# Optimization experiments

Hardware: AMD Instinct MI355X
Metric: run time of the kernel (lower is better)

The kernel has to match this reference:

```python
import jax, jax.numpy as jnp
import numpy as np

N_NODES = 50000
N_EDGES = 800000
IN_CH = 128
HEADS = 4
OUT_CH = 4
N_GRAPHS = 64
NEG_SLOPE = 0.2  # GATv2Conv default leaky_relu slope
EPS = 1e-5       # GraphNorm eps


def _seg_sum(x, seg, n):
    return jax.ops.segment_sum(x, seg, num_segments=n)


def _seg_mean(x, seg, n):
    s = _seg_sum(x, seg, n)
    cnt = _seg_sum(jnp.ones((seg.shape[0],), x.dtype), seg, n)
    return s / jnp.maximum(cnt, 1.0)[:, None]


def gatv2_conv(x, src, dst, n, w_l, w_r, att, bias, heads, out_ch, concat):
    # x: [N, F_in]; src/dst: [E_tot] (self-loops already appended)
    x_l = (x @ w_l).reshape(n, heads, out_ch)
    x_r = (x @ w_r).reshape(n, heads, out_ch)
    m = jax.nn.leaky_relu(x_l[src] + x_r[dst], NEG_SLOPE)   # [E, H, C]
    e = jnp.einsum('ehc,hc->eh', m, att)                    # [E, H]
    # softmax over incoming edges of each destination node
    e_max = jax.ops.segment_max(e, dst, num_segments=n)     # [N, H]
    w = jnp.exp(e - e_max[dst])
    denom = _seg_sum(w, dst, n)                             # [N, H]
    alpha = w / denom[dst]
    out = _seg_sum(alpha[:, :, None] * x_l[src], dst, n)    # [N, H, C]
    out = out.reshape(n, heads * out_ch) if concat else out.mean(axis=1)
    return out + bias


def graph_norm(x, batch, weight, bias, mean_scale, n_graphs):
    mu = _seg_mean(x, batch, n_graphs)                      # [G, C]
    out = x - mu[batch] * mean_scale
    var = _seg_mean(out * out, batch, n_graphs)
    return out / jnp.sqrt(var[batch] + EPS) * weight + bias


def setup_inputs() -> dict:
    key = jax.random.key(0)
    ks = jax.random.split(key, 20)
    H = HEADS
    d = {}
    d['x'] = jax.random.normal(ks[0], (N_NODES, IN_CH), dtype=jnp.float32)
    d['edge_index'] = jax.random.randint(ks[1], (2, N_EDGES), 0, N_NODES, dtype=jnp.int32)
    d['batch'] = jnp.sort(jax.random.randint(ks[2], (N_NODES,), 0, N_GRAPHS, dtype=jnp.int32))
    def glorot(k, shape):
        fan = shape[0] + shape[-1]
        return jax.random.normal(k, shape, dtype=jnp.float32) * np.sqrt(2.0 / fan).astype(np.float32)
    # layer 1: in 128 -> 32 per head, concat -> 128
    d['w_l1'] = glorot(ks[3], (IN_CH, H * 32)); d['w_r1'] = glorot(ks[4], (IN_CH, H * 32))
    d['att1'] = glorot(ks[5], (H, 32)); d['b1'] = jnp.zeros((H * 32,), jnp.float32)
    d['gn1_w'] = jnp.ones((H * 32,), jnp.float32); d['gn1_b'] = jnp.zeros((H * 32,), jnp.float32); d['gn1_s'] = jnp.ones((H * 32,), jnp.float32)
    # layer 2: 128 -> 16 per head, concat -> 64
    d['w_l2'] = glorot(ks[6], (H * 32, H * 16)); d['w_r2'] = glorot(ks[7], (H * 32, H * 16))
    d['att2'] = glorot(ks[8], (H, 16)); d['b2'] = jnp.zeros((H * 16,), jnp.float32)
    d['gn2_w'] = jnp.ones((H * 16,), jnp.float32); d['gn2_b'] = jnp.zeros((H * 16,), jnp.float32); d['gn2_s'] = jnp.ones((H * 16,), jnp.float32)
    # layer 3: 64 -> 8 per head, mean over heads -> 8
    d['w_l3'] = glorot(ks[9], (H * 16, H * 8)); d['w_r3'] = glorot(ks[10], (H * 16, H * 8))
    d['att3'] = glorot(ks[11], (H, 8)); d['b3'] = jnp.zeros((8,), jnp.float32)
    d['gn3_w'] = jnp.ones((8,), jnp.float32); d['gn3_b'] = jnp.zeros((8,), jnp.float32); d['gn3_s'] = jnp.ones((8,), jnp.float32)
    d['lin_w'] = glorot(ks[12], (8, OUT_CH)); d['lin_b'] = jnp.zeros((OUT_CH,), jnp.float32)
    return d


def reference(x, edge_index, batch,
              w_l1, w_r1, att1, b1, gn1_w, gn1_b, gn1_s,
              w_l2, w_r2, att2, b2, gn2_w, gn2_b, gn2_s,
              w_l3, w_r3, att3, b3, gn3_w, gn3_b, gn3_s,
              lin_w, lin_b):
    n = x.shape[0]
    loop = jnp.arange(n, dtype=edge_index.dtype)
    src = jnp.concatenate([edge_index[0], loop])  # add_self_loops=True (PyG default)
    dst = jnp.concatenate([edge_index[1], loop])
    h = gatv2_conv(x, src, dst, n, w_l1, w_r1, att1, b1, HEADS, 32, True)
    h = jax.nn.relu(graph_norm(h, batch, gn1_w, gn1_b, gn1_s, N_GRAPHS))
    h = gatv2_conv(h, src, dst, n, w_l2, w_r2, att2, b2, HEADS, 16, True)
    h = jax.nn.relu(graph_norm(h, batch, gn2_w, gn2_b, gn2_s, N_GRAPHS))
    h = gatv2_conv(h, src, dst, n, w_l3, w_r3, att3, b3, HEADS, 8, False)
    h = jax.nn.relu(graph_norm(h, batch, gn3_w, gn3_b, gn3_s, N_GRAPHS))
    features = _seg_mean(h, batch, N_GRAPHS)  # global_mean_pool -> [G, 8]
    logits = features @ lin_w + lin_b         # [G, OUT_CH]
    return (logits, features)
```

## Files before the change

kernel.cpp:

```cpp
#include <hip/hip_runtime.h>
#include <hip/hip_fp16.h>
#include <math.h>

#define NN 50000
#define NE 800000
#define ET (NE + NN)
#define NG 64
#define H 4
#define NBK 196
#define CH 2048
#define SB ((ET + CH - 1) / CH)
#define GD ((NN + 63) / 64)

typedef _Float16 half8 __attribute__((ext_vector_type(8)));
typedef _Float16 half4 __attribute__((ext_vector_type(4)));
typedef _Float16 hv2 __attribute__((ext_vector_type(2)));
typedef float floatx4 __attribute__((ext_vector_type(4)));


template <int K, int M2>
__device__ __forceinline__ void wprep_fn(int chunk, const float* __restrict__ Wl, const float* __restrict__ Wr,
                                         _Float16* __restrict__ Wfrag) {
    constexpr int MTOT = 2 * M2, NT = MTOT / 16;
    if (chunk >= MTOT * K / 8) return;
    int lane = chunk & 63, tt = chunk >> 6;
    int t = tt % NT, kt = tt / NT;
    int n = t * 16 + (lane & 15);
    int kb = kt * 32 + (lane >> 4) * 8;
    const float* src = (n < M2) ? (Wl + n) : (Wr + (n - M2));
    half8 h;
#pragma unroll
    for (int j = 0; j < 8; ++j) h[j] = (_Float16)src[(size_t)(kb + j) * M2];
    *(half8*)(Wfrag + (size_t)chunk * 8) = h;
}


__global__ __launch_bounds__(256) void k_prep(const float* __restrict__ Wl1, const float* __restrict__ Wr1,
                                              const float* __restrict__ Wl2, const float* __restrict__ Wr2,
                                              const float* __restrict__ Wl3, const float* __restrict__ Wr3,
                                              _Float16* __restrict__ Wf1, _Float16* __restrict__ Wf2,
                                              _Float16* __restrict__ Wf3,
                                              const int* __restrict__ batch, int* __restrict__ bpos,
                                              const int* __restrict__ ei, int* __restrict__ bcnt) {
    int b = blockIdx.x, t = threadIdx.x;
    if (b < 16) { wprep_fn<128, 128>(b * 256 + t, Wl1, Wr1, Wf1); return; }
    if (b < 24) { wprep_fn<128, 64>((b - 16) * 256 + t, Wl2, Wr2, Wf2); return; }
    if (b < 26) { wprep_fn<64, 32>((b - 24) * 256 + t, Wl3, Wr3, Wf3); return; }
    if (b < 26 + NBK) {
        int i = (b - 26) * 256 + t;
        if (i >= NN) return;
        int cur = batch[i];
        int prev = (i == 0) ? -1 : batch[i - 1];
        for (int g = prev + 1; g <= cur; ++g) bpos[g] = i;
        if (i == NN - 1)
            for (int g = cur + 1; g <= NG; ++g) bpos[g] = NN;
        return;
    }
    __shared__ int hist[NBK];
    int b0 = b - 26 - NBK;
    for (int i = t; i < NBK; i += 256) hist[i] = 0;
    __syncthreads();
#pragma unroll
    for (int pass = 0; pass < CH / 256; ++pass) {
        int e = b0 * CH + pass * 256 + t;
        if (e < ET) {
            int d = (e < NE) ? ei[NE + e] : (e - NE);
            atomicAdd(&hist[d >> 8], 1);
        }
    }
    __syncthreads();
    if (t < NBK) bcnt[t * SB + b0] = hist[t];
}


template <typename AT, bool NORM>
__device__ __forceinline__ half8 load_a8(const AT* __restrict__ ap, const float* pa, const float* pb) {
    if constexpr (NORM) {
        half8 raw = *(const half8*)ap;
        half8 h;
#pragma unroll
        for (int j = 0; j < 8; ++j) {
            float y = fmaf((float)raw[j], pa[j], pb[j]);
            h[j] = (_Float16)fmaxf(y, 0.f);
        }
        return h;
    } else if constexpr (__is_same(AT, _Float16)) {
        return *(const half8*)ap;
    } else {
        const float4* p = (const float4*)ap;
        float4 a = p[0], b = p[1];
        half8 h;
        h[0] = (_Float16)a.x; h[1] = (_Float16)a.y; h[2] = (_Float16)a.z; h[3] = (_Float16)a.w;
        h[4] = (_Float16)b.x; h[5] = (_Float16)b.y; h[6] = (_Float16)b.z; h[7] = (_Float16)b.w;
        return h;
    }
}

template <int K, int M2, typename AT, bool NORM>
__device__ __forceinline__ void dualgemm_body(int blk, int tid, const AT* __restrict__ Ain,
                                              const _Float16* __restrict__ Wfrag,
                                              __half* __restrict__ Ol, __half* __restrict__ Or,
                                              const float* __restrict__ gsum, const float* __restrict__ gsq,
                                              const float* __restrict__ gw, const float* __restrict__ gbb,
                                              const float* __restrict__ gms,
                                              const int* __restrict__ bpos, const int* __restrict__ batch) {
    constexpr int MTOT = 2 * M2;
    constexpr int NT = MTOT / 16;
    constexpr int KT = K / 32;
    constexpr int PK = NORM ? K : 1;
    __shared__ float spab[2][8][PK];
    int wid = tid >> 6, lane = tid & 63;
    int q = lane >> 4, l15 = lane & 15;
    int r0 = blk * 64 + wid * 16;
    int arow = min(r0 + l15, NN - 1);
    const AT* ap = Ain + (size_t)arow * K + q * 8;
    const float *pa = nullptr, *pb = nullptr;
    if constexpr (NORM) {
        int rb = blk * 64;
        int g0 = batch[min(rb, NN - 1)];
        int g1 = batch[min(rb + 63, NN - 1)];
        int gspan = min(g1 - g0 + 1, 8);
        for (int i = tid; i < gspan * K; i += 256) {
            int gg = i / K, c = i - gg * K;
            int g = g0 + gg;
            float cg = fmaxf((float)(bpos[g + 1] - bpos[g]), 1.f);
            float mu = gsum[(size_t)g * K + c] / cg;
            float ex2 = gsq[(size_t)g * K + c] / cg;
            float s_ = gms[c];
            float var = ex2 - s_ * (2.f - s_) * mu * mu;
            float a = rsqrtf(var + 1e-5f) * gw[c];
            spab[0][gg][c] = a;
            spab[1][gg][c] = gbb[c] - mu * s_ * a;
        }
        __syncthreads();
        int gg = min(batch[arow] - g0, 7);
        pa = &spab[0][gg][q * 8];
        pb = &spab[1][gg][q * 8];
    }

    floatx4 acc[NT];
#pragma unroll
    for (int t = 0; t < NT; ++t) acc[t] = (floatx4){0.f, 0.f, 0.f, 0.f};

#pragma unroll
    for (int kt = 0; kt < KT; ++kt) {
        half8 a8 = load_a8<AT, NORM>(ap + kt * 32, pa + (NORM ? kt * 32 : 0), pb + (NORM ? kt * 32 : 0));
        const _Float16* wp = Wfrag + ((size_t)(kt * NT) * 64 + lane) * 8;
#pragma unroll
        for (int t = 0; t < NT; ++t) {
            half8 b8 = *(const half8*)(wp + (size_t)t * 64 * 8);
            acc[t] = __builtin_amdgcn_mfma_f32_16x16x32_f16(a8, b8, acc[t], 0, 0, 0);
        }
    }

#pragma unroll
    for (int t = 0; t < NT; ++t) {
        int cn = t * 16 + l15;
#pragma unroll
        for (int reg = 0; reg < 4; ++reg) {
            int r = r0 + q * 4 + reg;
            if (r < NN) {
                if (cn < M2) Ol[(size_t)r * M2 + cn] = __float2half(acc[t][reg]);
                else         Or[(size_t)r * M2 + (cn - M2)] = __float2half(acc[t][reg]);
            }
        }
    }
}

template <int K, int M2>
__global__ __launch_bounds__(256) void k_dualgemm_n(const __half* __restrict__ Ain,
                                                    const _Float16* __restrict__ Wfrag,
                                                    __half* __restrict__ Ol, __half* __restrict__ Or,
                                                    const float* __restrict__ gsum, const float* __restrict__ gsq,
                                                    const float* __restrict__ gw, const float* __restrict__ gbb,
                                                    const float* __restrict__ gms,
                                                    const int* __restrict__ bpos, const int* __restrict__ batch) {
    dualgemm_body<K, M2, _Float16, true>(blockIdx.x, threadIdx.x, (const _Float16*)Ain, Wfrag, Ol, Or,
                                         gsum, gsq, gw, gbb, gms, bpos, batch);
}


__device__ __forceinline__ void bscanA_fn(int b, int t, const int* __restrict__ bcnt,
                                          int* __restrict__ boff, int* __restrict__ tot) {
    __shared__ int lds[256];
    int i0 = 2 * t, i1 = 2 * t + 1;
    int v0 = (i0 < SB) ? bcnt[b * SB + i0] : 0;
    int v1 = (i1 < SB) ? bcnt[b * SB + i1] : 0;
    int pair = v0 + v1;
    lds[t] = pair;
    __syncthreads();
    for (int off = 1; off < 256; off <<= 1) {
        int y = (t >= off) ? lds[t - off] : 0;
        __syncthreads();
        lds[t] += y;
        __syncthreads();
    }
    int excl = lds[t] - pair;
    if (i0 < SB) boff[b * SB + i0] = excl;
    if (i1 < SB) boff[b * SB + i1] = excl + v0;
    if (t == 255) tot[b] = lds[255];
}


__global__ __launch_bounds__(256) void k_gemm1_scan(const float* __restrict__ x, const _Float16* __restrict__ Wf1,
                                                    __half* __restrict__ Ol, __half* __restrict__ Or,
                                                    const int* __restrict__ bcnt, int* __restrict__ boff,
                                                    int* __restrict__ tot) {
    if (blockIdx.x < GD)
        dualgemm_body<128, 128, float, false>(blockIdx.x, threadIdx.x, x, Wf1, Ol, Or,
                                              nullptr, nullptr, nullptr, nullptr, nullptr, nullptr, nullptr);
    else
        bscanA_fn(blockIdx.x - GD, threadIdx.x, bcnt, boff, tot);
}


__device__ __forceinline__ void edge_sd(int e, const int* __restrict__ ei, int& s, int& d) {
    if (e < NE) { s = ei[e]; d = ei[NE + e]; } else { s = e - NE; d = s; }
}

__global__ __launch_bounds__(256) void k_bscatter(const int* __restrict__ ei, const int* __restrict__ tot,
                                                  const int* __restrict__ boff, unsigned int* __restrict__ ebuf) {
    __shared__ int eb[256];
    __shared__ int cur[NBK];
    int b0 = blockIdx.x, t = threadIdx.x;
    int v = (t < NBK) ? tot[t] : 0;
    eb[t] = v;
    __syncthreads();
    for (int off = 1; off < 256; off <<= 1) {
        int y = (t >= off) ? eb[t - off] : 0;
        __syncthreads();
        eb[t] += y;
        __syncthreads();
    }
    if (t < NBK) cur[t] = (eb[t] - v) + boff[t * SB + b0];
    __syncthreads();
#pragma unroll
    for (int pass = 0; pass < CH / 256; ++pass) {
        int e = b0 * CH + pass * 256 + t;
        if (e < ET) {
            int s, d;
            edge_sd(e, ei, s, d);
            int pos = atomicAdd(&cur[d >> 8], 1);
            ebuf[pos] = ((unsigned)s << 16) | (unsigned)(d & 255);
        }
    }
}


__global__ __launch_bounds__(256) void k_bsort(const unsigned int* __restrict__ ebuf,
                                               const int* __restrict__ tot,
                                               int* __restrict__ rowptr, unsigned short* __restrict__ colsrc) {
    __shared__ int eb[256];
    __shared__ int sbase;
    __shared__ int cnt2[256];
    __shared__ int sc[256];
    __shared__ int cur2[256];
    int b = blockIdx.x, t = threadIdx.x;
    int v = (t < NBK) ? tot[t] : 0;
    eb[t] = v;
    __syncthreads();
    for (int off = 1; off < 256; off <<= 1) {
        int y = (t >= off) ? eb[t - off] : 0;
        __syncthreads();
        eb[t] += y;
        __syncthreads();
    }
    if (t == b) sbase = eb[t] - v;
    __syncthreads();
    int base = sbase, n = tot[b];
    cnt2[t] = 0;
    __syncthreads();
    for (int i = t; i < n; i += 256) atomicAdd(&cnt2[ebuf[base + i] & 255], 1);
    __syncthreads();
    int cv = cnt2[t];
    sc[t] = cv;
    __syncthreads();
    for (int off = 1; off < 256; off <<= 1) {
        int y = (t >= off) ? sc[t - off] : 0;
        __syncthreads();
        sc[t] += y;
        __syncthreads();
    }
    int excl = sc[t] - cv;
    int d = b * 256 + t;
    if (d < NN) rowptr[d] = base + excl;
    if (b == 0 && t == 0) rowptr[NN] = ET;
    cur2[t] = excl;
    __syncthreads();
    for (int i = t; i < n; i += 256) {
        unsigned u = ebuf[base + i];
        int pos = atomicAdd(&cur2[u & 255], 1);
        colsrc[base + pos] = (unsigned short)(u >> 16);
    }
}


template <int CP> struct HVec { hv2 h2[CP / 2]; };

template <int CP>
__device__ __forceinline__ HVec<CP> load_hv(const __half* __restrict__ p) {
    HVec<CP> r;
    if constexpr (CP == 16) {
        float4* rp = (float4*)&r;
        rp[0] = ((const float4*)p)[0];
        rp[1] = ((const float4*)p)[1];
    } else if constexpr (CP == 8) {
        float4 t = *(const float4*)p; r = *(HVec<CP>*)&t;
    } else if constexpr (CP == 4) {
        float2 t = *(const float2*)p; r = *(HVec<CP>*)&t;
    } else {
        r.h2[0] = *(const hv2*)p;
    }
    return r;
}

template <int C, int EP, bool CONCAT>
__global__ __launch_bounds__(256) void k_attn(const __half* __restrict__ xl, const __half* __restrict__ xr,
                                              const int* __restrict__ rowptr,
                                              const unsigned short* __restrict__ colsrc,
                                              const float* __restrict__ att, const float* __restrict__ bias,
                                              __half* __restrict__ out) {
    constexpr int CP = C / EP;
    constexpr int LEP = (EP == 4) ? 2 : ((EP == 2) ? 1 : 0);
    int t = blockIdx.x * 256 + threadIdx.x;
    int part = t & (EP - 1);
    int nh = t >> LEP;
    if (nh >= NN * H) return;
    int node = nh >> 2, h = nh & 3;
    int cbase = h * C + part * CP;
    hv2 xrr2[CP / 2], attv2[CP / 2];
    float acc[CP];
    {
        HVec<CP> xrv = load_hv<CP>(xr + (size_t)node * (H * C) + cbase);
        const float* q = att + cbase;
#pragma unroll
        for (int j = 0; j < CP / 2; ++j) {
            xrr2[j] = xrv.h2[j];
            attv2[j] = (hv2){(_Float16)q[2 * j], (_Float16)q[2 * j + 1]};
        }
#pragma unroll
        for (int c = 0; c < CP; ++c) acc[c] = 0.f;
    }
    float denom = 0.f;
    int beg = rowptr[node], end = rowptr[node + 1];

    auto process = [&](const HVec<CP>& xv) {
        float part_s = 0.f;
#pragma unroll
        for (int j = 0; j < CP / 2; ++j) {
            hv2 z = xv.h2[j] + xrr2[j];
            hv2 l = __builtin_elementwise_max(z, z * (_Float16)0.2f);
            part_s = __builtin_amdgcn_fdot2(l, attv2[j], part_s, false);
        }
        float score = part_s;
#pragma unroll
        for (int mask = 1; mask < EP; mask <<= 1) score += __shfl_xor(score, mask, 64);
        float w = __expf(score);
        denom += w;
        const _Float16* xh = (const _Float16*)&xv;
#pragma unroll
        for (int c = 0; c < CP; ++c) acc[c] = fmaf(w, (float)xh[c], acc[c]);
    };

    int idx = beg;
    for (; idx + 8 <= end; idx += 8) {
        int s[8];
#pragma unroll
        for (int u = 0; u < 8; ++u) s[u] = colsrc[idx + u];
        HVec<CP> xv[8];
#pragma unroll
        for (int u = 0; u < 8; ++u) xv[u] = load_hv<CP>(xl + (size_t)s[u] * (H * C) + cbase);
#pragma unroll
        for (int u = 0; u < 8; ++u) process(xv[u]);
    }
    for (; idx + 4 <= end; idx += 4) {
        int s0 = colsrc[idx], s1 = colsrc[idx + 1], s2 = colsrc[idx + 2], s3 = colsrc[idx + 3];
        HVec<CP> xv0 = load_hv<CP>(xl + (size_t)s0 * (H * C) + cbase);
        HVec<CP> xv1 = load_hv<CP>(xl + (size_t)s1 * (H * C) + cbase);
        HVec<CP> xv2 = load_hv<CP>(xl + (size_t)s2 * (H * C) + cbase);
        HVec<CP> xv3 = load_hv<CP>(xl + (size_t)s3 * (H * C) + cbase);
        process(xv0);
        process(xv1);
        process(xv2);
        process(xv3);
    }
    for (; idx < end; ++idx) {
        int s = colsrc[idx];
        HVec<CP> xv = load_hv<CP>(xl + (size_t)s * (H * C) + cbase);
        process(xv);
    }

    float inv = 1.f / denom;
    _Float16* op = (_Float16*)out + (size_t)node * (H * C) + cbase;
    _Float16 hv[CP];
#pragma unroll
    for (int c = 0; c < CP; ++c) {
        float v = acc[c] * inv;
        if (CONCAT) v += bias[cbase + c];
        hv[c] = (_Float16)v;
    }
    if constexpr (CP >= 8) {
#pragma unroll
        for (int j = 0; j < CP / 8; ++j) *(half8*)(op + 8 * j) = *(half8*)(hv + 8 * j);
    } else if constexpr (CP == 4) {
        *(half4*)op = *(half4*)hv;
    } else {
        *(hv2*)op = *(hv2*)hv;
    }
}


template <int LOGC, int SPLIT>
__global__ __launch_bounds__(256) void k_gnred2(const __half* __restrict__ h, const int* __restrict__ bpos,
                                                float* __restrict__ sum, float* __restrict__ sumsq) {
    constexpr int C = 1 << LOGC;
    constexpr int RG = 256 >> LOGC;
    int g = blockIdx.x / SPLIT, s = blockIdx.x % SPLIT;
    int c = threadIdx.x & (C - 1);
    int rg = threadIdx.x >> LOGC;
    int b0 = bpos[g], b1 = bpos[g + 1];
    int n = b1 - b0;
    int seg = (n + SPLIT - 1) / SPLIT;
    int r0 = b0 + s * seg;
    int r1 = min(r0 + seg, b1);
    float sv = 0.f, ssv = 0.f;
    for (int r = r0 + rg; r < r1; r += RG) {
        float x = __half2float(h[(size_t)r * C + c]);
        sv += x; ssv += x * x;
    }
    __shared__ float ls[256], lss[256];
    ls[threadIdx.x] = sv; lss[threadIdx.x] = ssv;
    __syncthreads();
    for (int off = 128; off >= C; off >>= 1) {
        if (threadIdx.x < off) {
            ls[threadIdx.x] += ls[threadIdx.x + off];
            lss[threadIdx.x] += lss[threadIdx.x + off];
        }
        __syncthreads();
    }
    if (threadIdx.x < C) {
        atomicAdd(&sum[g * C + threadIdx.x], ls[threadIdx.x]);
        atomicAdd(&sumsq[g * C + threadIdx.x], lss[threadIdx.x]);
    }
}


template <int SPLIT>
__global__ __launch_bounds__(256) void k_headgn(const __half* __restrict__ tmp, const float* __restrict__ b3,
                                                const int* __restrict__ bpos, float* __restrict__ Af,
                                                float* __restrict__ sum, float* __restrict__ sumsq) {
    constexpr int C = 8, RG = 32;
    int g = blockIdx.x / SPLIT, s = blockIdx.x % SPLIT;
    int c = threadIdx.x & 7;
    int rg = threadIdx.x >> 3;
    int b0 = bpos[g], b1 = bpos[g + 1];
    int n = b1 - b0;
    int seg = (n + SPLIT - 1) / SPLIT;
    int r0 = b0 + s * seg;
    int r1 = min(r0 + seg, b1);
    float bias = b3[c];
    float sv = 0.f, ssv = 0.f;
    for (int r = r0 + rg; r < r1; r += RG) {
        const __half* p = tmp + (size_t)r * 32 + c;
        float v = 0.25f * (__half2float(p[0]) + __half2float(p[8]) +
                           __half2float(p[16]) + __half2float(p[24])) + bias;
        Af[(size_t)r * C + c] = v;
        sv += v; ssv += v * v;
    }
    __shared__ float ls[256], lss[256];
    ls[threadIdx.x] = sv; lss[threadIdx.x] = ssv;
    __syncthreads();
    for (int off = 128; off >= C; off >>= 1) {
        if (threadIdx.x < off) {
            ls[threadIdx.x] += ls[threadIdx.x + off];
            lss[threadIdx.x] += lss[threadIdx.x + off];
        }
        __syncthreads();
    }
    if (threadIdx.x < C) {
        atomicAdd(&sum[g * C + threadIdx.x], ls[threadIdx.x]);
        atomicAdd(&sumsq[g * C + threadIdx.x], lss[threadIdx.x]);
    }
}


__global__ __launch_bounds__(256) void k_gnpool_final(const float* __restrict__ Af, const int* __restrict__ bpos,
                                                      const float* __restrict__ sum, const float* __restrict__ sumsq,
                                                      const float* __restrict__ w,
                                                      const float* __restrict__ b, const float* __restrict__ ms,
                                                      const float* __restrict__ lw, const float* __restrict__ lb,
                                                      float* __restrict__ outp) {
    constexpr int C = 8, RG = 32;
    int g = blockIdx.x;
    int c = threadIdx.x & 7;
    int rg = threadIdx.x >> 3;
    int b0 = bpos[g], b1 = bpos[g + 1];
    int n = b1 - b0;
    float cg = fmaxf((float)n, 1.f);
    float mu = sum[g * C + c] / cg;
    float ex2 = sumsq[g * C + c] / cg;
    float s_ = ms[c];
    float var = ex2 - (2.f * s_ - s_ * s_) * mu * mu;
    float rs = rsqrtf(var + 1e-5f) * w[c];
    float bb = b[c], mus = mu * s_;
    float pv = 0.f;
    for (int r = b0 + rg; r < b1; r += RG) {
        float y = fmaxf((Af[(size_t)r * C + c] - mus) * rs + bb, 0.f);
        pv += y;
    }
    __shared__ float ls[256];
    __shared__ float feat[8];
    ls[threadIdx.x] = pv;
    __syncthreads();
    for (int off = 128; off >= C; off >>= 1) {
        if (threadIdx.x < off) ls[threadIdx.x] += ls[threadIdx.x + off];
        __syncthreads();
    }
    if (threadIdx.x < C) {
        float f = ls[threadIdx.x] / cg;
        feat[threadIdx.x] = f;
        outp[256 + g * 8 + threadIdx.x] = f;
    }
    __syncthreads();
    if (threadIdx.x < 4) {
        float a = lb[threadIdx.x];
#pragma unroll
        for (int cc = 0; cc < 8; ++cc) a += feat[cc] * lw[cc * 4 + threadIdx.x];
        outp[g * 4 + threadIdx.x] = a;
    }
}


extern "C" void kernel_launch(void* const* d_in, const int* in_sizes, int n_in,
                              void* d_out, int out_size, void* d_ws, size_t ws_size,
                              hipStream_t stream) {
    const float* x    = (const float*)d_in[0];
    const int*   ei   = (const int*)d_in[1];
    const int*   batch= (const int*)d_in[2];
    const float *w_l1 = (const float*)d_in[3],  *w_r1 = (const float*)d_in[4];
    const float *att1 = (const float*)d_in[5],  *b1   = (const float*)d_in[6];
    const float *gn1w = (const float*)d_in[7],  *gn1b = (const float*)d_in[8],  *gn1s = (const float*)d_in[9];
    const float *w_l2 = (const float*)d_in[10], *w_r2 = (const float*)d_in[11];
    const float *att2 = (const float*)d_in[12], *b2   = (const float*)d_in[13];
    const float *gn2w = (const float*)d_in[14], *gn2b = (const float*)d_in[15], *gn2s = (const float*)d_in[16];
    const float *w_l3 = (const float*)d_in[17], *w_r3 = (const float*)d_in[18];
    const float *att3 = (const float*)d_in[19], *b3   = (const float*)d_in[20];
    const float *gn3w = (const float*)d_in[21], *gn3b = (const float*)d_in[22], *gn3s = (const float*)d_in[23];
    const float *lw   = (const float*)d_in[24], *lb   = (const float*)d_in[25];

    char* ws = (char*)d_ws;
    size_t off = 0;
    auto alloc = [&](size_t bytes) -> void* {
        void* p = ws + off;
        off += (bytes + 255) & ~(size_t)255;
        return p;
    };
    __half* Ah  = (__half*)alloc((size_t)NN * 128 * 2);
    __half* Bh  = (__half*)alloc((size_t)NN * 128 * 2);
    __half* Chh = (__half*)alloc((size_t)NN * 64 * 2);
    __half* B   = (__half*)alloc((size_t)NN * 128 * 2);
    __half* Cb  = (__half*)alloc((size_t)NN * 64 * 2);
    float*  Af  = (float*)alloc((size_t)NN * 8 * 4);
    _Float16* Wf1 = (_Float16*)alloc((size_t)256 * 128 * 2);
    _Float16* Wf2 = (_Float16*)alloc((size_t)128 * 128 * 2);
    _Float16* Wf3 = (_Float16*)alloc((size_t)64 * 64 * 2);
    int* rowptr = (int*)alloc((size_t)(NN + 1) * 4);
    unsigned short* colsrc = (unsigned short*)alloc((size_t)ET * 2);
    unsigned int* ebuf = (unsigned int*)alloc((size_t)ET * 4);
    int* bcnt   = (int*)alloc((size_t)NBK * SB * 4);
    int* boff   = (int*)alloc((size_t)NBK * SB * 4);
    int* tot    = (int*)alloc((size_t)NBK * 4);
    int* bpos   = (int*)alloc((size_t)(NG + 1) * 4);
    char* zbase = ws + off;
    float* sum1 = (float*)alloc((size_t)NG * 128 * 4);
    float* sq1  = (float*)alloc((size_t)NG * 128 * 4);
    float* sum2 = (float*)alloc((size_t)NG * 64 * 4);
    float* sq2  = (float*)alloc((size_t)NG * 64 * 4);
    float* sum3 = (float*)alloc((size_t)NG * 8 * 4);
    float* sq3  = (float*)alloc((size_t)NG * 8 * 4);
    size_t zbytes = (size_t)((ws + off) - zbase);
    (void)hipMemsetAsync(zbase, 0, zbytes, stream);

    k_prep<<<26 + NBK + SB, 256, 0, stream>>>(w_l1, w_r1, w_l2, w_r2, w_l3, w_r3, Wf1, Wf2, Wf3,
                                              batch, bpos, ei, bcnt);
    k_gemm1_scan<<<GD + NBK, 256, 0, stream>>>(x, Wf1, Ah, B, bcnt, boff, tot);
    k_bscatter<<<SB, 256, 0, stream>>>(ei, tot, boff, ebuf);
    k_bsort<<<NBK, 256, 0, stream>>>(ebuf, tot, rowptr, colsrc);

    int gA2ep = (NN * H * 2 + 255) / 256;
    int gA1ep = (NN * H + 255) / 256;

    k_attn<32, 2, true><<<gA2ep, 256, 0, stream>>>(Ah, B, rowptr, colsrc, att1, b1, Bh);
    k_gnred2<7, 8><<<NG * 8, 256, 0, stream>>>(Bh, bpos, sum1, sq1);

    k_dualgemm_n<128, 64><<<GD, 256, 0, stream>>>(Bh, Wf2, Ah, Cb, sum1, sq1, gn1w, gn1b, gn1s, bpos, batch);
    k_attn<16, 2, true><<<gA2ep, 256, 0, stream>>>(Ah, Cb, rowptr, colsrc, att2, b2, Chh);
    k_gnred2<6, 8><<<NG * 8, 256, 0, stream>>>(Chh, bpos, sum2, sq2);

    k_dualgemm_n<64, 32><<<GD, 256, 0, stream>>>(Chh, Wf3, Ah, B, sum2, sq2, gn2w, gn2b, gn2s, bpos, batch);
    k_attn<8, 1, false><<<gA1ep, 256, 0, stream>>>(Ah, B, rowptr, colsrc, att3, nullptr, Bh);
    k_headgn<8><<<NG * 8, 256, 0, stream>>>(Bh, b3, bpos, Af, sum3, sq3);
    k_gnpool_final<<<NG, 256, 0, stream>>>(Af, bpos, sum3, sq3, gn3w, gn3b, gn3s, lw, lb, (float*)d_out);
}
```

Baseline: 297.8 us.

## Reorder attention nodes by in-degree to balance per-wavefront work

```diff
diff --git a/kernel.cpp b/kernel.cpp
--- a/kernel.cpp
+++ b/kernel.cpp
@@ -249,7 +249,8 @@
 
 __global__ __launch_bounds__(256) void k_bsort(const unsigned int* __restrict__ ebuf,
                                                const int* __restrict__ tot,
-                                               int* __restrict__ rowptr, unsigned short* __restrict__ colsrc) {
+                                               int* __restrict__ rowptr, unsigned short* __restrict__ colsrc,
+                                               int* __restrict__ dhist) {
     __shared__ int eb[256];
     __shared__ int sbase;
     __shared__ int cnt2[256];
@@ -283,7 +284,10 @@
     }
     int excl = sc[t] - cv;
     int d = b * 256 + t;
-    if (d < NN) rowptr[d] = base + excl;
+    if (d < NN) {
+        rowptr[d] = base + excl;
+        atomicAdd(&dhist[min(cv, 255)], 1);
+    }
     if (b == 0 && t == 0) rowptr[NN] = ET;
     cur2[t] = excl;
     __syncthreads();
@@ -291,6 +295,31 @@
         unsigned u = ebuf[base + i];
         int pos = atomicAdd(&cur2[u & 255], 1);
         colsrc[base + pos] = (unsigned short)(u >> 16);
+    }
+}
+
+
+__global__ __launch_bounds__(256) void k_perm(const int* __restrict__ rowptr, const int* __restrict__ dhist,
+                                              int* __restrict__ gcur, int* __restrict__ perm) {
+    __shared__ int scan[256];
+    __shared__ int base[256];
+    int t = threadIdx.x;
+    int own = dhist[t];
+    scan[t] = own;
+    __syncthreads();
+    for (int off = 1; off < 256; off <<= 1) {
+        int y = (t >= off) ? scan[t - off] : 0;
+        __syncthreads();
+        scan[t] += y;
+        __syncthreads();
+    }
+    base[t] = scan[t] - own;
+    __syncthreads();
+    int i = blockIdx.x * 256 + t;
+    if (i < NN) {
+        int d = min(rowptr[i + 1] - rowptr[i], 255);
+        int pos = base[d] + atomicAdd(&gcur[d], 1);
+        perm[pos] = i;
     }
 }
 
@@ -318,6 +347,7 @@
 __global__ __launch_bounds__(256) void k_attn(const __half* __restrict__ xl, const __half* __restrict__ xr,
                                               const int* __restrict__ rowptr,
                                               const unsigned short* __restrict__ colsrc,
+                                              const int* __restrict__ perm,
                                               const float* __restrict__ att, const float* __restrict__ bias,
                                               __half* __restrict__ out) {
     constexpr int CP = C / EP;
@@ -326,7 +356,8 @@
     int part = t & (EP - 1);
     int nh = t >> LEP;
     if (nh >= NN * H) return;
-    int node = nh >> 2, h = nh & 3;
+    int node = perm[nh >> 2];
+    int h = nh & 3;
     int cbase = h * C + part * CP;
     hv2 xrr2[CP / 2], attv2[CP / 2];
     float acc[CP];
@@ -571,6 +602,7 @@
     int* boff   = (int*)alloc((size_t)NBK * SB * 4);
     int* tot    = (int*)alloc((size_t)NBK * 4);
     int* bpos   = (int*)alloc((size_t)(NG + 1) * 4);
+    int* perm   = (int*)alloc((size_t)NN * 4);
     char* zbase = ws + off;
     float* sum1 = (float*)alloc((size_t)NG * 128 * 4);
     float* sq1  = (float*)alloc((size_t)NG * 128 * 4);
@@ -578,6 +610,8 @@
     float* sq2  = (float*)alloc((size_t)NG * 64 * 4);
     float* sum3 = (float*)alloc((size_t)NG * 8 * 4);
     float* sq3  = (float*)alloc((size_t)NG * 8 * 4);
+    int* dhist  = (int*)alloc((size_t)256 * 4);
+    int* gcur   = (int*)alloc((size_t)256 * 4);
     size_t zbytes = (size_t)((ws + off) - zbase);
     (void)hipMemsetAsync(zbase, 0, zbytes, stream);
 
@@ -585,20 +619,21 @@
                                               batch, bpos, ei, bcnt);
     k_gemm1_scan<<<GD + NBK, 256, 0, stream>>>(x, Wf1, Ah, B, bcnt, boff, tot);
     k_bscatter<<<SB, 256, 0, stream>>>(ei, tot, boff, ebuf);
-    k_bsort<<<NBK, 256, 0, stream>>>(ebuf, tot, rowptr, colsrc);
+    k_bsort<<<NBK, 256, 0, stream>>>(ebuf, tot, rowptr, colsrc, dhist);
+    k_perm<<<NBK, 256, 0, stream>>>(rowptr, dhist, gcur, perm);
 
     int gA2ep = (NN * H * 2 + 255) / 256;
     int gA1ep = (NN * H + 255) / 256;
 
-    k_attn<32, 2, true><<<gA2ep, 256, 0, stream>>>(Ah, B, rowptr, colsrc, att1, b1, Bh);
+    k_attn<32, 2, true><<<gA2ep, 256, 0, stream>>>(Ah, B, rowptr, colsrc, perm, att1, b1, Bh);
     k_gnred2<7, 8><<<NG * 8, 256, 0, stream>>>(Bh, bpos, sum1, sq1);
 
     k_dualgemm_n<128, 64><<<GD, 256, 0, stream>>>(Bh, Wf2, Ah, Cb, sum1, sq1, gn1w, gn1b, gn1s, bpos, batch);
-    k_attn<16, 2, true><<<gA2ep, 256, 0, stream>>>(Ah, Cb, rowptr, colsrc, att2, b2, Chh);
+    k_attn<16, 2, true><<<gA2ep, 256, 0, stream>>>(Ah, Cb, rowptr, colsrc, perm, att2, b2, Chh);
     k_gnred2<6, 8><<<NG * 8, 256, 0, stream>>>(Chh, bpos, sum2, sq2);
 
     k_dualgemm_n<64, 32><<<GD, 256, 0, stream>>>(Chh, Wf3, Ah, B, sum2, sq2, gn2w, gn2b, gn2s, bpos, batch);
-    k_attn<8, 1, false><<<gA1ep, 256, 0, stream>>>(Ah, B, rowptr, colsrc, att3, nullptr, Bh);
+    k_attn<8, 1, false><<<gA1ep, 256, 0, stream>>>(Ah, B, rowptr, colsrc, perm, att3, nullptr, Bh);
     k_headgn<8><<<NG * 8, 256, 0, stream>>>(Bh, b3, bpos, Af, sum3, sq3);
     k_gnpool_final<<<NG, 256, 0, stream>>>(Af, bpos, sum3, sq3, gn3w, gn3b, gn3s, lw, lb, (float*)d_out);
 }
```

Measured after the change: 572.2 us. +92.2%, slower.
